# Performance work log

Hardware: AMD Instinct MI355X
Metric: run time of the kernel (lower is better)

## Reference

```python
import math
import jax, jax.numpy as jnp
import numpy as np

B, DIM, C, N = 1024, 512, 1000, 8
R = 0.05
WEIGHT_LAMBDA = 0.3
CN = C * N
TOPK = math.ceil(R * CN)  # 400


def setup_inputs() -> dict:
    key = jax.random.key(0)
    k1, k2, k3 = jax.random.split(key, 3)
    x = jax.random.normal(k1, (B, DIM), dtype=jnp.float32)
    # kaiming_uniform_(a=sqrt(5)) on a (DIM, CN) tensor: fan_in = CN (torch 2D fan_in = size(1)),
    # gain = sqrt(2/(1+a^2)) = sqrt(1/3), bound = gain * sqrt(3/fan_in)
    bound = math.sqrt(1.0 / 3.0) * math.sqrt(3.0 / CN)
    proxies = jax.random.uniform(k2, (DIM, CN), dtype=jnp.float32, minval=-bound, maxval=bound)
    target = jax.random.randint(k3, (B,), 0, C)
    return {"x": x, "proxies": proxies, "target": target}


def reference(x, proxies, target):
    instance_label = jnp.repeat(jnp.arange(C), N)  # (CN,)

    # F.normalize(Proxies, p=2, dim=0) with eps=1e-12 clamp
    norm = jnp.maximum(jnp.linalg.norm(proxies, axis=0, keepdims=True), 1e-12)
    centers = proxies / norm  # (DIM, CN)

    similarity = x @ centers  # (B, CN)

    positive_mask = (target[:, None] == instance_label[None, :]).astype(similarity.dtype)

    # topk over similarity boosted so all positives are included, then scatter 1s
    _, idx = jax.lax.top_k(similarity + 1000.0 * positive_mask, TOPK)  # (B, TOPK)
    mask = jnp.zeros_like(similarity).at[jnp.arange(B)[:, None], idx].set(1.0)
    mask = jax.lax.stop_gradient(mask)

    prob_a = mask * similarity  # (B, CN)
    # matmul with block one-hot y_instance_onehot == sum over the N proxies of each class
    logits = prob_a.reshape(B, C, N).sum(axis=-1)  # (B, C)

    logits_mask = jax.lax.stop_gradient((logits != 0.0).astype(logits.dtype))
    exp_l = jnp.exp(logits) * logits_mask
    predict = exp_l / (1e-8 + exp_l.sum(axis=1, keepdims=True))

    # sum(-y_onehot * log(predict+1e-20), 1) == -log(predict[b, target[b]] + 1e-20)
    loss_classify = jnp.mean(-jnp.log(predict[jnp.arange(B), target] + 1e-20))

    # regularizer: (centers.T @ centers) @ y_instance_onehot, fused as
    # centers.T @ (per-class sum of centers) -- identical math, avoids the CNxCN matrix
    centers_cls = centers.reshape(DIM, C, N).sum(axis=-1)  # (DIM, C)
    centers_logits = centers.T @ centers_cls  # (CN, C)
    logp = jax.nn.log_softmax(centers_logits, axis=1)
    reg = -jnp.mean(logp[jnp.arange(CN), instance_label])

    total = loss_classify + WEIGHT_LAMBDA * reg
    return (total, loss_classify)
```

## Files before the change

kernel.cpp:

```cpp
#include <hip/hip_runtime.h>
#include <hip/hip_bf16.h>
#include <math.h>

#define PB   1024
#define PDIM 512
#define PC   1000
#define PN   8
#define PCN  8000
#define PTOPK 400
#define NONPOS_K 392
#define NBIN 1024
#define CANDMAX 1024

typedef __bf16 bf16x8 __attribute__((ext_vector_type(8)));
typedef __bf16 bf16x4 __attribute__((ext_vector_type(4)));
typedef float  f32x4  __attribute__((ext_vector_type(4)));

__device__ static inline void async_load16(const __bf16* g, __bf16* l) {
    __builtin_amdgcn_global_load_lds(
        (const __attribute__((address_space(1))) void*)g,
        (__attribute__((address_space(3))) void*)l,
        16, 0, 0);
}

__global__ __launch_bounds__(256) void k_pre(const float* __restrict__ x,
                                             const float* __restrict__ P,
                                             __bf16* __restrict__ xb,
                                             float* __restrict__ ssqp,
                                             float* __restrict__ esd,
                                             float* __restrict__ padf,
                                             float* __restrict__ acc) {
    int b = blockIdx.x, tid = threadIdx.x;
    if (b == 0 && tid < 8) acc[tid] = 0.f;
    if (b < 512) {
        int i = b * 256 + tid;
        float4 v = ((const float4*)x)[i];
        bf16x4 o;
        o[0] = (__bf16)v.x; o[1] = (__bf16)v.y; o[2] = (__bf16)v.z; o[3] = (__bf16)v.w;
        ((bf16x4*)xb)[i] = o;
    } else if (b < 768) {
        int idx = b - 512;
        int slice = idx & 7, jb = idx >> 3;
        int j = jb * 256 + tid;
        if (j < PCN) {
            const float* p = P + (size_t)(slice * 64) * PCN + j;
            float ss = 0.f;
#pragma unroll 8
            for (int r = 0; r < 64; ++r) {
                float v = p[(size_t)r * PCN];
                ss = fmaf(v, v, ss);
            }
            ssqp[slice * PCN + j] = ss;
        }
    } else {
        int i = (b - 768) * 256 + tid;
        if (i < 16000) esd[i] = 0.f;
        else if (i < 16000 + 6144) padf[i - 16000] = 0.f;
    }
}

__global__ __launch_bounds__(256) void k_tpose(const float* __restrict__ P,
                                               const float* __restrict__ ssqp,
                                               __bf16* __restrict__ Pt,
                                               __bf16* __restrict__ ccls) {
    __shared__ float t[64][65];
    __shared__ float sinv[64];
    int tid = threadIdx.x;
    int tx = tid & 63, ty = tid >> 6;
    int j0 = blockIdx.x * 64, d0 = blockIdx.y * 64;
    if (tid < 64) {
        float sq = 0.f;
#pragma unroll
        for (int p2 = 0; p2 < 8; ++p2) sq += ssqp[p2 * PCN + j0 + tid];
        sinv[tid] = 1.0f / fmaxf(sqrtf(sq), 1e-12f);
    }
#pragma unroll
    for (int r = 0; r < 16; ++r) {
        int d = d0 + ty * 16 + r;
        t[ty * 16 + r][tx] = P[(size_t)d * PCN + j0 + tx];
    }
    __syncthreads();
    float cs0 = 0.f, cs1 = 0.f;
#pragma unroll
    for (int r = 0; r < 16; ++r) {
        int jl = ty * 16 + r;
        float val = t[tx][jl] * sinv[jl];
        Pt[(size_t)(j0 + jl) * PDIM + d0 + tx] = (__bf16)val;
        if (r < 8) cs0 += val; else cs1 += val;
    }
    int c0 = (j0 >> 3) + ty * 2;
    ccls[(size_t)c0 * PDIM + d0 + tx] = (__bf16)cs0;
    ccls[(size_t)(c0 + 1) * PDIM + d0 + tx] = (__bf16)cs1;
}

__global__ __launch_bounds__(512, 2) void k_gemms2(const __bf16* __restrict__ xb,
                                                   const __bf16* __restrict__ Pt,
                                                   const __bf16* __restrict__ ccls,
                                                   __bf16* __restrict__ simb,
                                                   float* __restrict__ esum,
                                                   float* __restrict__ diag) {
    __shared__ __align__(16) __bf16 As[2][256 * 64];
    __shared__ __align__(16) __bf16 Bs[2][256 * 64];

    int tid = threadIdx.x;
    int w = tid >> 6, lane = tid & 63;
    int wr = w >> 2, wc = w & 3;
    int quad = lane >> 4, l15 = lane & 15;

    int bid = blockIdx.x;
    bool is_sim = bid < 128;
    int M0, N0, Amax, Bmax;
    const __bf16 *Ab, *Bb;
    if (is_sim) {
        int mt = bid >> 5, nt = bid & 31;
        M0 = mt * 256; N0 = nt * 256;
        Ab = xb; Bb = Pt; Amax = PB - 1; Bmax = PCN - 1;
    } else {
        int b2 = bid - 128;
        int mt = b2 >> 2, nt = b2 & 3;
        M0 = mt * 256; N0 = nt * 256;
        Ab = Pt; Bb = ccls; Amax = PCN - 1; Bmax = 1023;
    }

    f32x4 acc[8][4] = {};

#define STAGE(kt_) {                                                         \
    int k0_ = (kt_) * 64, bb_ = (kt_) & 1;                                   \
    _Pragma("unroll")                                                        \
    for (int p_ = 0; p_ < 4; ++p_) {                                         \
        int idx_ = p_ * 512 + tid;                                           \
        int row_ = idx_ >> 3, sp_ = idx_ & 7;                                \
        int gk_ = ((sp_ ^ (row_ & 7)) << 3) + k0_;                           \
        int ga_ = M0 + row_; if (ga_ > Amax) ga_ = Amax;                     \
        async_load16(Ab + (size_t)ga_ * PDIM + gk_, &As[bb_][idx_ * 8]);     \
        int gb_ = N0 + row_; if (gb_ > Bmax) gb_ = Bmax;                     \
        async_load16(Bb + (size_t)gb_ * PDIM + gk_, &Bs[bb_][idx_ * 8]);     \
    } }

    STAGE(0)
    for (int kt = 0; kt < 8; ++kt) {
        int cur = kt & 1;
        asm volatile("s_waitcnt lgkmcnt(0)" ::: "memory");
        __builtin_amdgcn_s_barrier();
        if (kt < 7) {
            STAGE(kt + 1)
            asm volatile("s_waitcnt vmcnt(8)" ::: "memory");
        } else {
            asm volatile("s_waitcnt vmcnt(0)" ::: "memory");
        }
        __builtin_amdgcn_s_barrier();

#pragma unroll
        for (int ks = 0; ks < 2; ++ks) {
            bf16x8 af[8], bfr[4];
#pragma unroll
            for (int mi = 0; mi < 8; ++mi) {
                int row = wr * 128 + mi * 16 + l15;
                af[mi] = *(const bf16x8*)&As[cur][(row << 6) +
                         ((((ks << 2) + quad) ^ (row & 7)) << 3)];
            }
#pragma unroll
            for (int nj = 0; nj < 4; ++nj) {
                int row = wc * 64 + nj * 16 + l15;
                bfr[nj] = *(const bf16x8*)&Bs[cur][(row << 6) +
                          ((((ks << 2) + quad) ^ (row & 7)) << 3)];
            }
            __builtin_amdgcn_s_setprio(1);
#pragma unroll
            for (int mi = 0; mi < 8; ++mi)
#pragma unroll
                for (int nj = 0; nj < 4; ++nj)
                    acc[mi][nj] = __builtin_amdgcn_mfma_f32_16x16x32_bf16(
                        af[mi], bfr[nj], acc[mi][nj], 0, 0, 0);
            __builtin_amdgcn_s_setprio(0);
        }
    }
#undef STAGE

    if (is_sim) {
#pragma unroll
        for (int mi = 0; mi < 8; ++mi) {
            int r0 = M0 + wr * 128 + mi * 16 + quad * 4;
#pragma unroll
            for (int nj = 0; nj < 4; ++nj) {
                int cc = N0 + wc * 64 + nj * 16 + l15;
                if (cc < PCN) {
#pragma unroll
                    for (int r = 0; r < 4; ++r)
                        simb[(size_t)(r0 + r) * PCN + cc] = (__bf16)acc[mi][nj][r];
                }
            }
        }
    } else {
#pragma unroll
        for (int mi = 0; mi < 8; ++mi) {
            int r0 = M0 + wr * 128 + mi * 16 + quad * 4;
            float psum[4] = {0.f, 0.f, 0.f, 0.f};
#pragma unroll
            for (int nj = 0; nj < 4; ++nj) {
                int cc = N0 + wc * 64 + nj * 16 + l15;
                bool cvalid = (cc < PC);
#pragma unroll
                for (int r = 0; r < 4; ++r) {
                    float v = acc[mi][nj][r];
                    psum[r] += cvalid ? expf(v) : 0.f;
                    int rr = r0 + r;
                    if (cvalid && rr < PCN && cc == (rr >> 3)) diag[rr] = v;
                }
            }
#pragma unroll
            for (int off = 1; off < 16; off <<= 1)
#pragma unroll
                for (int r = 0; r < 4; ++r)
                    psum[r] += __shfl_xor(psum[r], off, 64);
            if (l15 == 0) {
#pragma unroll
                for (int r = 0; r < 4; ++r) {
                    int rr = r0 + r;
                    if (rr < PCN) atomicAdd(&esum[rr], psum[r]);
                }
            }
        }
    }
}

__global__ __launch_bounds__(256) void k_rowloss(const __bf16* __restrict__ sim,
                                                 const int* __restrict__ target,
                                                 float* __restrict__ acc) {
    __shared__ unsigned hist[NBIN];
    __shared__ float redf[8];
    __shared__ unsigned wtot[4];
    __shared__ float cand[CANDMAX];
    __shared__ unsigned candn;
    __shared__ int s_bin, s_A;
    __shared__ float s_tau;
    __shared__ int s_gt, s_eq;
    __shared__ float s_et;

    int b = blockIdx.x, tid = threadIdx.x;
    int lane = tid & 63, wv = tid >> 6;
    const bf16x8* row8 = (const bf16x8*)(sim + (size_t)b * PCN);
    int targ = target[b];

#pragma unroll
    for (int k = 0; k < 4; ++k) hist[tid + 256 * k] = 0u;
    if (tid == 0) candn = 0u;

    float pv[4][8];
    float lmn = INFINITY, lmx = -INFINITY;
#pragma unroll
    for (int k = 0; k < 4; ++k) {
        int c = tid + 256 * k;
        if (c < PC) {
            bf16x8 vv = row8[c];
#pragma unroll
            for (int n = 0; n < 8; ++n) pv[k][n] = (float)vv[n];
            if (c != targ) {
#pragma unroll
                for (int n = 0; n < 8; ++n) {
                    lmn = fminf(lmn, pv[k][n]);
                    lmx = fmaxf(lmx, pv[k][n]);
                }
            }
        } else {
#pragma unroll
            for (int n = 0; n < 8; ++n) pv[k][n] = 0.f;
        }
    }
    for (int off = 32; off; off >>= 1) {
        lmn = fminf(lmn, __shfl_down(lmn, off, 64));
        lmx = fmaxf(lmx, __shfl_down(lmx, off, 64));
    }
    if (lane == 0) { redf[wv] = lmn; redf[4 + wv] = lmx; }
    __syncthreads();
    float lo = fminf(fminf(redf[0], redf[1]), fminf(redf[2], redf[3]));
    float hi = fmaxf(fmaxf(redf[4], redf[5]), fmaxf(redf[6], redf[7]));
    float range = hi - lo;
    float scale = (range > 0.f) ? (float)NBIN / range : 0.f;

#pragma unroll
    for (int k = 0; k < 4; ++k) {
        int c = tid + 256 * k;
        if (c < PC && c != targ) {
#pragma unroll
            for (int n = 0; n < 8; ++n) {
                int bin = (int)((pv[k][n] - lo) * scale);
                bin = bin < 0 ? 0 : (bin > NBIN - 1 ? NBIN - 1 : bin);
                atomicAdd(&hist[bin], 1u);
            }
        }
    }
    __syncthreads();

    int b0 = tid * 4;
    unsigned h0 = hist[b0], h1 = hist[b0 + 1], h2 = hist[b0 + 2], h3 = hist[b0 + 3];
    unsigned l3 = h3, l2 = h2 + l3, l1 = h1 + l2, l0 = h0 + l1;
    unsigned T = l0;
#pragma unroll
    for (int step = 1; step < 64; step <<= 1) {
        unsigned u = __shfl_down(T, step, 64);
        if (lane + step < 64) T += u;
    }
    if (lane == 0) wtot[wv] = T;
    __syncthreads();
    unsigned tail = 0;
#pragma unroll
    for (int w2 = 0; w2 < 4; ++w2) if (w2 > wv) tail += wtot[w2];
    unsigned E = T - l0 + tail;
    {
        unsigned sfx[4] = {l0 + E, l1 + E, l2 + E, l3 + E};
        unsigned nxt[4] = {l1 + E, l2 + E, l3 + E, E};
#pragma unroll
        for (int i = 0; i < 4; ++i)
            if (sfx[i] >= NONPOS_K && nxt[i] < NONPOS_K) {
                s_bin = b0 + i;
                s_A = (int)nxt[i];
            }
    }
    __syncthreads();
    int tbin = s_bin, A = s_A;

#pragma unroll
    for (int k = 0; k < 4; ++k) {
        int c = tid + 256 * k;
        if (c < PC && c != targ) {
#pragma unroll
            for (int n = 0; n < 8; ++n) {
                int bin = (int)((pv[k][n] - lo) * scale);
                bin = bin < 0 ? 0 : (bin > NBIN - 1 ? NBIN - 1 : bin);
                if (bin == tbin) {
                    unsigned idx = atomicAdd(&candn, 1u);
                    if (idx < CANDMAX) cand[idx] = pv[k][n];
                }
            }
        }
    }
    __syncthreads();
    int m = (int)candn; if (m > CANDMAX) m = CANDMAX;
    int rank = NONPOS_K - A;
    for (int ci = tid; ci < m; ci += 256) {
        float val = cand[ci];
        int g = 0, e = 0;
        for (int i = 0; i < m; ++i) {
            g += cand[i] > val;
            e += cand[i] == val;
        }
        if (g < rank && rank <= g + e) { s_tau = val; s_gt = g; s_eq = e; }
    }
    __syncthreads();
    float tau = s_tau;
    int cgt = A + s_gt, ceq = s_eq;
    int rem = NONPOS_K - cgt;
    bool all_eq = (rem >= ceq);

    int offs[4] = {0, 0, 0, 0};
    if (!all_eq) {
        unsigned chunk_base = 0;
#pragma unroll
        for (int k = 0; k < 4; ++k) {
            int c = tid + 256 * k;
            unsigned tn = 0;
            if (c < PC && c != targ) {
#pragma unroll
                for (int n = 0; n < 8; ++n) tn += (pv[k][n] == tau) ? 1u : 0u;
            }
            unsigned inc = tn;
#pragma unroll
            for (int step = 1; step < 64; step <<= 1) {
                unsigned u = __shfl_up(inc, step, 64);
                if (lane >= step) inc += u;
            }
            __syncthreads();
            if (lane == 63) wtot[wv] = inc;
            __syncthreads();
            unsigned base = 0;
#pragma unroll
            for (int w2 = 0; w2 < 4; ++w2) if (w2 < wv) base += wtot[w2];
            offs[k] = (int)(chunk_base + base + inc - tn);
            chunk_base += wtot[0] + wtot[1] + wtot[2] + wtot[3];
        }
    }

    float psum = 0.f;
#pragma unroll
    for (int k = 0; k < 4; ++k) {
        int c = tid + 256 * k;
        if (c >= PC) continue;
        float lg = 0.f;
        if (c == targ) {
#pragma unroll
            for (int n = 0; n < 8; ++n) lg += pv[k][n];
        } else {
#pragma unroll
            for (int n = 0; n < 8; ++n) {
                float v = pv[k][n];
                bool sel = v > tau;
                if (!sel && v == tau) {
                    if (all_eq) sel = true;
                    else { sel = (offs[k] < rem); offs[k]++; }
                }
                if (sel) lg += v;
            }
        }
        float e = (lg != 0.0f) ? expf(lg) : 0.0f;
        psum += e;
        if (c == targ) s_et = e;
    }
    for (int off = 32; off; off >>= 1) psum += __shfl_down(psum, off, 64);
    if (lane == 0) redf[wv] = psum;
    __syncthreads();
    if (tid == 0) {
        float denom = 1e-8f + redf[0] + redf[1] + redf[2] + redf[3];
        atomicAdd(acc, -logf(s_et / denom + 1e-20f));
    }
}

__global__ __launch_bounds__(256) void k_final(const float* __restrict__ esum,
                                               const float* __restrict__ diag,
                                               const float* __restrict__ acc,
                                               float* __restrict__ out) {
    __shared__ float redf[4];
    int tid = threadIdx.x, lane = tid & 63, wv = tid >> 6;
    float s = 0.f;
    for (int j = tid; j < PCN; j += 256)
        s += logf(esum[j]) - diag[j];
    for (int off = 32; off; off >>= 1) s += __shfl_down(s, off, 64);
    if (lane == 0) redf[wv] = s;
    __syncthreads();
    if (tid == 0) {
        float rg = (redf[0] + redf[1] + redf[2] + redf[3]) * (1.0f / PCN);
        float lc = acc[0] * (1.0f / PB);
        out[0] = lc + 0.3f * rg;
        out[1] = lc;
    }
}

extern "C" void kernel_launch(void* const* d_in, const int* in_sizes, int n_in,
                              void* d_out, int out_size, void* d_ws, size_t ws_size,
                              hipStream_t stream) {
    const float* x       = (const float*)d_in[0];
    const float* proxies = (const float*)d_in[1];
    const int*   target  = (const int*)d_in[2];
    float* out = (float*)d_out;
    float* ws  = (float*)d_ws;

    float*  acc   = ws;
    float*  ssqp  = ws + 64;
    float*  esum  = ws + 64064;
    float*  diag  = ws + 72064;
    __bf16* xb    = (__bf16*)(ws + 80064);
    __bf16* cclsb = (__bf16*)(ws + 342208);
    __bf16* Pt    = (__bf16*)(ws + 604352);
    __bf16* simb  = (__bf16*)(ws + 2652352);

    float* padf = (float*)cclsb + 256000;

    k_pre<<<856, 256, 0, stream>>>(x, proxies, xb, ssqp, esum, padf, acc);
    k_tpose<<<dim3(125, 8), 256, 0, stream>>>(proxies, ssqp, Pt, cclsb);

    k_gemms2<<<256, 512, 0, stream>>>(xb, Pt, cclsb, simb, esum, diag);

    k_rowloss<<<PB, 256, 0, stream>>>(simb, target, acc);
    k_final<<<1, 256, 0, stream>>>(esum, diag, acc, out);
}
```

Baseline: 138.6 us.

## Fuse prep kernels, pack bf16 sim stores, fold final reduction into rowloss

Merges the norm, transpose and convert kernels into one prep kernel, where each of 125 blocks computes the column norms for 64 proxies and then transposes all 8 DIM chunks itself. The final loss reduction moves into the last k_rowloss block through a completion counter, which removes a launch. GEMM similarity stores now pair adjacent bf16 values with a lane shuffle so each write is 32 bits. The trade-off is that the prep stage runs on only 125 blocks doing serial transpose work, which could become a bottleneck.

Result: slower. 203.3 us (+46.6%).

```diff
diff --git a/kernel.cpp b/kernel.cpp
--- a/kernel.cpp
+++ b/kernel.cpp
@@ -23,74 +23,75 @@
         16, 0, 0);
 }
 
-__global__ __launch_bounds__(256) void k_pre(const float* __restrict__ x,
-                                             const float* __restrict__ P,
-                                             __bf16* __restrict__ xb,
-                                             float* __restrict__ ssqp,
-                                             float* __restrict__ esd,
-                                             float* __restrict__ padf,
-                                             float* __restrict__ acc) {
-    int b = blockIdx.x, tid = threadIdx.x;
-    if (b == 0 && tid < 8) acc[tid] = 0.f;
-    if (b < 512) {
-        int i = b * 256 + tid;
+__device__ static inline unsigned bf16bits(float v) {
+    __bf16 b = (__bf16)v;
+    unsigned short u;
+    __builtin_memcpy(&u, &b, 2);
+    return (unsigned)u;
+}
+
+__global__ __launch_bounds__(256) void k_prep(const float* __restrict__ x,
+                                              const float* __restrict__ P,
+                                              __bf16* __restrict__ xb,
+                                              __bf16* __restrict__ Pt,
+                                              __bf16* __restrict__ ccls,
+                                              float* __restrict__ esd,
+                                              float* __restrict__ padf,
+                                              float* __restrict__ acc) {
+    int bid = blockIdx.x, tid = threadIdx.x;
+    if (bid < 125) {
+        __shared__ float t[64][65];
+        __shared__ float red[4][64];
+        __shared__ float sinv[64];
+        int j0 = bid * 64;
+        int tx = tid & 63, ty = tid >> 6;
+        {
+            const float* pc = P + (size_t)(ty * 128) * PCN + j0 + tx;
+            float ss = 0.f;
+#pragma unroll 8
+            for (int k = 0; k < 128; ++k) {
+                float v = pc[(size_t)k * PCN];
+                ss = fmaf(v, v, ss);
+            }
+            red[ty][tx] = ss;
+        }
+        __syncthreads();
+        if (tid < 64) {
+            float sq = red[0][tid] + red[1][tid] + red[2][tid] + red[3][tid];
+            sinv[tid] = 1.0f / fmaxf(sqrtf(sq), 1e-12f);
+        }
+        for (int dc = 0; dc < 8; ++dc) {
+            __syncthreads();
+#pragma unroll
+            for (int rr = 0; rr < 16; ++rr) {
+                int d = dc * 64 + ty * 16 + rr;
+                t[ty * 16 + rr][tx] = P[(size_t)d * PCN + j0 + tx];
+            }
+            __syncthreads();
+            float cs0 = 0.f, cs1 = 0.f;
+#pragma unroll
+            for (int rr = 0; rr < 16; ++rr) {
+                int jj = ty * 16 + rr;
+                float val = t[tx][jj] * sinv[jj];
+                Pt[(size_t)(j0 + jj) * PDIM + dc * 64 + tx] = (__bf16)val;
+                if (rr < 8) cs0 += val; else cs1 += val;
+            }
+            int c0 = (j0 >> 3) + ty * 2;
+            ccls[(size_t)c0 * PDIM + dc * 64 + tx] = (__bf16)cs0;
+            ccls[(size_t)(c0 + 1) * PDIM + dc * 64 + tx] = (__bf16)cs1;
+        }
+    } else if (bid < 637) {
+        int i = (bid - 125) * 256 + tid;
         float4 v = ((const float4*)x)[i];
         bf16x4 o;
         o[0] = (__bf16)v.x; o[1] = (__bf16)v.y; o[2] = (__bf16)v.z; o[3] = (__bf16)v.w;
         ((bf16x4*)xb)[i] = o;
-    } else if (b < 768) {
-        int idx = b - 512;
-        int slice = idx & 7, jb = idx >> 3;
-        int j = jb * 256 + tid;
-        if (j < PCN) {
-            const float* p = P + (size_t)(slice * 64) * PCN + j;
-            float ss = 0.f;
-#pragma unroll 8
-            for (int r = 0; r < 64; ++r) {
-                float v = p[(size_t)r * PCN];
-                ss = fmaf(v, v, ss);
-            }
-            ssqp[slice * PCN + j] = ss;
-        }
     } else {
-        int i = (b - 768) * 256 + tid;
+        if (bid == 637 && tid < 16) acc[tid] = 0.f;
+        int i = (bid - 637) * 256 + tid;
         if (i < 16000) esd[i] = 0.f;
         else if (i < 16000 + 6144) padf[i - 16000] = 0.f;
     }
-}
-
-__global__ __launch_bounds__(256) void k_tpose(const float* __restrict__ P,
-                                               const float* __restrict__ ssqp,
-                                               __bf16* __restrict__ Pt,
-                                               __bf16* __restrict__ ccls) {
-    __shared__ float t[64][65];
-    __shared__ float sinv[64];
-    int tid = threadIdx.x;
-    int tx = tid & 63, ty = tid >> 6;
-    int j0 = blockIdx.x * 64, d0 = blockIdx.y * 64;
-    if (tid < 64) {
-        float sq = 0.f;
-#pragma unroll
-        for (int p2 = 0; p2 < 8; ++p2) sq += ssqp[p2 * PCN + j0 + tid];
-        sinv[tid] = 1.0f / fmaxf(sqrtf(sq), 1e-12f);
-    }
-#pragma unroll
-    for (int r = 0; r < 16; ++r) {
-        int d = d0 + ty * 16 + r;
-        t[ty * 16 + r][tx] = P[(size_t)d * PCN + j0 + tx];
-    }
-    __syncthreads();
-    float cs0 = 0.f, cs1 = 0.f;
-#pragma unroll
-    for (int r = 0; r < 16; ++r) {
-        int jl = ty * 16 + r;
-        float val = t[tx][jl] * sinv[jl];
-        Pt[(size_t)(j0 + jl) * PDIM + d0 + tx] = (__bf16)val;
-        if (r < 8) cs0 += val; else cs1 += val;
-    }
-    int c0 = (j0 >> 3) + ty * 2;
-    ccls[(size_t)c0 * PDIM + d0 + tx] = (__bf16)cs0;
-    ccls[(size_t)(c0 + 1) * PDIM + d0 + tx] = (__bf16)cs1;
 }
 
 __global__ __launch_bounds__(512, 2) void k_gemms2(const __bf16* __restrict__ xb,
@@ -184,10 +185,12 @@
 #pragma unroll
             for (int nj = 0; nj < 4; ++nj) {
                 int cc = N0 + wc * 64 + nj * 16 + l15;
-                if (cc < PCN) {
-#pragma unroll
-                    for (int r = 0; r < 4; ++r)
-                        simb[(size_t)(r0 + r) * PCN + cc] = (__bf16)acc[mi][nj][r];
+#pragma unroll
+                for (int r = 0; r < 4; ++r) {
+                    unsigned p = bf16bits(acc[mi][nj][r]);
+                    unsigned q = (unsigned)__shfl_xor((int)p, 1, 64);
+                    if (((l15 & 1) == 0) && cc < PCN)
+                        *(unsigned*)&simb[(size_t)(r0 + r) * PCN + cc] = p | (q << 16);
                 }
             }
         }
@@ -226,7 +229,10 @@
 
 __global__ __launch_bounds__(256) void k_rowloss(const __bf16* __restrict__ sim,
                                                  const int* __restrict__ target,
-                                                 float* __restrict__ acc) {
+                                                 float* __restrict__ acc,
+                                                 const float* __restrict__ esum,
+                                                 const float* __restrict__ diag,
+                                                 float* __restrict__ out) {
     __shared__ unsigned hist[NBIN];
     __shared__ float redf[8];
     __shared__ unsigned wtot[4];
@@ -236,6 +242,7 @@
     __shared__ float s_tau;
     __shared__ int s_gt, s_eq;
     __shared__ float s_et;
+    __shared__ unsigned s_rank2;
 
     int b = blockIdx.x, tid = threadIdx.x;
     int lane = tid & 63, wv = tid >> 6;
@@ -413,25 +420,24 @@
         float denom = 1e-8f + redf[0] + redf[1] + redf[2] + redf[3];
         atomicAdd(acc, -logf(s_et / denom + 1e-20f));
     }
-}
-
-__global__ __launch_bounds__(256) void k_final(const float* __restrict__ esum,
-                                               const float* __restrict__ diag,
-                                               const float* __restrict__ acc,
-                                               float* __restrict__ out) {
-    __shared__ float redf[4];
-    int tid = threadIdx.x, lane = tid & 63, wv = tid >> 6;
-    float s = 0.f;
-    for (int j = tid; j < PCN; j += 256)
-        s += logf(esum[j]) - diag[j];
-    for (int off = 32; off; off >>= 1) s += __shfl_down(s, off, 64);
-    if (lane == 0) redf[wv] = s;
-    __syncthreads();
-    if (tid == 0) {
-        float rg = (redf[0] + redf[1] + redf[2] + redf[3]) * (1.0f / PCN);
-        float lc = acc[0] * (1.0f / PB);
-        out[0] = lc + 0.3f * rg;
-        out[1] = lc;
+
+    __threadfence();
+    if (tid == 0) s_rank2 = atomicAdd((unsigned*)(acc + 8), 1u);
+    __syncthreads();
+    if (s_rank2 == PB - 1) {
+        float s = 0.f;
+        for (int j = tid; j < PCN; j += 256)
+            s += logf(esum[j]) - diag[j];
+        for (int off = 32; off; off >>= 1) s += __shfl_down(s, off, 64);
+        __syncthreads();
+        if (lane == 0) redf[wv] = s;
+        __syncthreads();
+        if (tid == 0) {
+            float rg = (redf[0] + redf[1] + redf[2] + redf[3]) * (1.0f / PCN);
+            float lc = atomicAdd(acc, 0.0f) * (1.0f / PB);
+            out[0] = lc + 0.3f * rg;
+            out[1] = lc;
+        }
     }
 }
 
@@ -445,7 +451,6 @@
     float* ws  = (float*)d_ws;
 
     float*  acc   = ws;
-    float*  ssqp  = ws + 64;
     float*  esum  = ws + 64064;
     float*  diag  = ws + 72064;
     __bf16* xb    = (__bf16*)(ws + 80064);
@@ -455,11 +460,7 @@
 
     float* padf = (float*)cclsb + 256000;
 
-    k_pre<<<856, 256, 0, stream>>>(x, proxies, xb, ssqp, esum, padf, acc);
-    k_tpose<<<dim3(125, 8), 256, 0, stream>>>(proxies, ssqp, Pt, cclsb);
-
+    k_prep<<<725, 256, 0, stream>>>(x, proxies, xb, Pt, cclsb, esum, padf, acc);
     k_gemms2<<<256, 512, 0, stream>>>(xb, Pt, cclsb, simb, esum, diag);
-
-    k_rowloss<<<PB, 256, 0, stream>>>(simb, target, acc);
-    k_final<<<1, 256, 0, stream>>>(esum, diag, acc, out);
-}
+    k_rowloss<<<PB, 256, 0, stream>>>(simb, target, acc, esum, diag, out);
+}
```

## Use exact bf16 radix-key histogram for top-k threshold and pack sim stores

Applied to the files above, without the earlier changes.

Replaces the min/max-range float histogram with a two-level radix select over the 16-bit order-preserving key of bf16 values. This drops the min/max reduction and the O(m^2) candidate ranking loop. It also merges the four tie-offset prefix scans into one scan of packed 16-bit counts and switches expf to __expf. In the GEMM epilogue, adjacent bf16 similarity values are paired with a lane shuffle so each store writes 32 bits, halving the store count.

Result: no change. 140.5 us (+1.3%).

```diff
diff --git a/kernel.cpp b/kernel.cpp
--- a/kernel.cpp
+++ b/kernel.cpp
@@ -10,7 +10,6 @@
 #define PTOPK 400
 #define NONPOS_K 392
 #define NBIN 1024
-#define CANDMAX 1024
 
 typedef __bf16 bf16x8 __attribute__((ext_vector_type(8)));
 typedef __bf16 bf16x4 __attribute__((ext_vector_type(4)));
@@ -21,6 +20,26 @@
         (const __attribute__((address_space(1))) void*)g,
         (__attribute__((address_space(3))) void*)l,
         16, 0, 0);
+}
+
+__device__ static inline unsigned bf16bits(float v) {
+    __bf16 b = (__bf16)v;
+    unsigned short u;
+    __builtin_memcpy(&u, &b, 2);
+    return (unsigned)u;
+}
+
+__device__ static inline unsigned bkey(float v) {
+    unsigned u = bf16bits(v);
+    return (u & 0x8000u) ? ((~u) & 0xffffu) : (u | 0x8000u);
+}
+
+__device__ static inline float keyf(unsigned t) {
+    unsigned bits = (t & 0x8000u) ? ((t & 0x7fffu) << 16)
+                                  : ((~t & 0xffffu) << 16);
+    float f;
+    __builtin_memcpy(&f, &bits, 4);
+    return f;
 }
 
 __global__ __launch_bounds__(256) void k_pre(const float* __restrict__ x,
@@ -184,10 +203,12 @@
 #pragma unroll
             for (int nj = 0; nj < 4; ++nj) {
                 int cc = N0 + wc * 64 + nj * 16 + l15;
-                if (cc < PCN) {
-#pragma unroll
-                    for (int r = 0; r < 4; ++r)
-                        simb[(size_t)(r0 + r) * PCN + cc] = (__bf16)acc[mi][nj][r];
+#pragma unroll
+                for (int r = 0; r < 4; ++r) {
+                    unsigned p = bf16bits(acc[mi][nj][r]);
+                    unsigned q = (unsigned)__shfl_xor((int)p, 1, 64);
+                    if (((l15 & 1) == 0) && cc < PCN)
+                        *(unsigned*)&simb[(size_t)(r0 + r) * PCN + cc] = p | (q << 16);
                 }
             }
         }
@@ -228,13 +249,11 @@
                                                  const int* __restrict__ target,
                                                  float* __restrict__ acc) {
     __shared__ unsigned hist[NBIN];
-    __shared__ float redf[8];
+    __shared__ unsigned hist2[64];
+    __shared__ float redf[4];
     __shared__ unsigned wtot[4];
-    __shared__ float cand[CANDMAX];
-    __shared__ unsigned candn;
-    __shared__ int s_bin, s_A;
-    __shared__ float s_tau;
-    __shared__ int s_gt, s_eq;
+    __shared__ unsigned wtot2[4][2];
+    __shared__ unsigned s_cb, s_A, s_tauk, s_gt, s_eq;
     __shared__ float s_et;
 
     int b = blockIdx.x, tid = threadIdx.x;
@@ -244,52 +263,32 @@
 
 #pragma unroll
     for (int k = 0; k < 4; ++k) hist[tid + 256 * k] = 0u;
-    if (tid == 0) candn = 0u;
+    if (tid < 64) hist2[tid] = 0u;
 
     float pv[4][8];
-    float lmn = INFINITY, lmx = -INFINITY;
+    bool msk[4];
 #pragma unroll
     for (int k = 0; k < 4; ++k) {
         int c = tid + 256 * k;
+        msk[k] = (c < PC) && (c != targ);
         if (c < PC) {
             bf16x8 vv = row8[c];
 #pragma unroll
             for (int n = 0; n < 8; ++n) pv[k][n] = (float)vv[n];
-            if (c != targ) {
-#pragma unroll
-                for (int n = 0; n < 8; ++n) {
-                    lmn = fminf(lmn, pv[k][n]);
-                    lmx = fmaxf(lmx, pv[k][n]);
-                }
-            }
         } else {
 #pragma unroll
             for (int n = 0; n < 8; ++n) pv[k][n] = 0.f;
         }
     }
-    for (int off = 32; off; off >>= 1) {
-        lmn = fminf(lmn, __shfl_down(lmn, off, 64));
-        lmx = fmaxf(lmx, __shfl_down(lmx, off, 64));
-    }
-    if (lane == 0) { redf[wv] = lmn; redf[4 + wv] = lmx; }
-    __syncthreads();
-    float lo = fminf(fminf(redf[0], redf[1]), fminf(redf[2], redf[3]));
-    float hi = fmaxf(fmaxf(redf[4], redf[5]), fmaxf(redf[6], redf[7]));
-    float range = hi - lo;
-    float scale = (range > 0.f) ? (float)NBIN / range : 0.f;
-
-#pragma unroll
-    for (int k = 0; k < 4; ++k) {
-        int c = tid + 256 * k;
-        if (c < PC && c != targ) {
-#pragma unroll
-            for (int n = 0; n < 8; ++n) {
-                int bin = (int)((pv[k][n] - lo) * scale);
-                bin = bin < 0 ? 0 : (bin > NBIN - 1 ? NBIN - 1 : bin);
-                atomicAdd(&hist[bin], 1u);
-            }
-        }
-    }
+    __syncthreads();
+
+#pragma unroll
+    for (int k = 0; k < 4; ++k)
+        if (msk[k]) {
+#pragma unroll
+            for (int n = 0; n < 8; ++n)
+                atomicAdd(&hist[bkey(pv[k][n]) >> 6], 1u);
+        }
     __syncthreads();
 
     int b0 = tid * 4;
@@ -313,72 +312,78 @@
 #pragma unroll
         for (int i = 0; i < 4; ++i)
             if (sfx[i] >= NONPOS_K && nxt[i] < NONPOS_K) {
-                s_bin = b0 + i;
-                s_A = (int)nxt[i];
-            }
-    }
-    __syncthreads();
-    int tbin = s_bin, A = s_A;
-
-#pragma unroll
-    for (int k = 0; k < 4; ++k) {
-        int c = tid + 256 * k;
-        if (c < PC && c != targ) {
+                s_cb = (unsigned)(b0 + i);
+                s_A = nxt[i];
+            }
+    }
+    __syncthreads();
+    unsigned cb = s_cb, A = s_A;
+
+#pragma unroll
+    for (int k = 0; k < 4; ++k)
+        if (msk[k]) {
 #pragma unroll
             for (int n = 0; n < 8; ++n) {
-                int bin = (int)((pv[k][n] - lo) * scale);
-                bin = bin < 0 ? 0 : (bin > NBIN - 1 ? NBIN - 1 : bin);
-                if (bin == tbin) {
-                    unsigned idx = atomicAdd(&candn, 1u);
-                    if (idx < CANDMAX) cand[idx] = pv[k][n];
-                }
-            }
-        }
-    }
-    __syncthreads();
-    int m = (int)candn; if (m > CANDMAX) m = CANDMAX;
-    int rank = NONPOS_K - A;
-    for (int ci = tid; ci < m; ci += 256) {
-        float val = cand[ci];
-        int g = 0, e = 0;
-        for (int i = 0; i < m; ++i) {
-            g += cand[i] > val;
-            e += cand[i] == val;
-        }
-        if (g < rank && rank <= g + e) { s_tau = val; s_gt = g; s_eq = e; }
-    }
-    __syncthreads();
-    float tau = s_tau;
-    int cgt = A + s_gt, ceq = s_eq;
-    int rem = NONPOS_K - cgt;
-    bool all_eq = (rem >= ceq);
+                unsigned kk = bkey(pv[k][n]);
+                if ((kk >> 6) == cb) atomicAdd(&hist2[kk & 63u], 1u);
+            }
+        }
+    __syncthreads();
+
+    if (wv == 0) {
+        unsigned h = hist2[lane];
+        unsigned sfx = h;
+#pragma unroll
+        for (int step = 1; step < 64; step <<= 1) {
+            unsigned u = __shfl_down(sfx, step, 64);
+            if (lane + step < 64) sfx += u;
+        }
+        unsigned nxt = sfx - h;
+        if (A + sfx >= NONPOS_K && A + nxt < NONPOS_K) {
+            s_tauk = (cb << 6) | (unsigned)lane;
+            s_gt = A + nxt;
+            s_eq = h;
+        }
+    }
+    __syncthreads();
+    float tauf = keyf(s_tauk);
+    int rem = NONPOS_K - (int)s_gt;
+    bool all_eq = (rem >= (int)s_eq);
 
     int offs[4] = {0, 0, 0, 0};
     if (!all_eq) {
-        unsigned chunk_base = 0;
+        unsigned tn[4];
 #pragma unroll
         for (int k = 0; k < 4; ++k) {
-            int c = tid + 256 * k;
-            unsigned tn = 0;
-            if (c < PC && c != targ) {
-#pragma unroll
-                for (int n = 0; n < 8; ++n) tn += (pv[k][n] == tau) ? 1u : 0u;
-            }
-            unsigned inc = tn;
-#pragma unroll
-            for (int step = 1; step < 64; step <<= 1) {
-                unsigned u = __shfl_up(inc, step, 64);
-                if (lane >= step) inc += u;
-            }
-            __syncthreads();
-            if (lane == 63) wtot[wv] = inc;
-            __syncthreads();
-            unsigned base = 0;
-#pragma unroll
-            for (int w2 = 0; w2 < 4; ++w2) if (w2 < wv) base += wtot[w2];
-            offs[k] = (int)(chunk_base + base + inc - tn);
-            chunk_base += wtot[0] + wtot[1] + wtot[2] + wtot[3];
-        }
+            unsigned t = 0;
+            if (msk[k]) {
+#pragma unroll
+                for (int n = 0; n < 8; ++n) t += (pv[k][n] == tauf) ? 1u : 0u;
+            }
+            tn[k] = t;
+        }
+        unsigned p01 = tn[0] | (tn[1] << 16), p23 = tn[2] | (tn[3] << 16);
+        unsigned i01 = p01, i23 = p23;
+#pragma unroll
+        for (int step = 1; step < 64; step <<= 1) {
+            unsigned u0 = __shfl_up(i01, step, 64);
+            unsigned u1 = __shfl_up(i23, step, 64);
+            if (lane >= step) { i01 += u0; i23 += u1; }
+        }
+        if (lane == 63) { wtot2[wv][0] = i01; wtot2[wv][1] = i23; }
+        __syncthreads();
+        unsigned base01 = 0, base23 = 0, t01 = 0, t23 = 0;
+#pragma unroll
+        for (int w2 = 0; w2 < 4; ++w2) {
+            if (w2 < wv) { base01 += wtot2[w2][0]; base23 += wtot2[w2][1]; }
+            t01 += wtot2[w2][0]; t23 += wtot2[w2][1];
+        }
+        unsigned e01 = i01 - p01, e23 = i23 - p23;
+        unsigned tot0 = t01 & 0xffffu, tot1 = t01 >> 16, tot2 = t23 & 0xffffu;
+        offs[0] = (int)((base01 & 0xffffu) + (e01 & 0xffffu));
+        offs[1] = (int)(tot0 + (base01 >> 16) + (e01 >> 16));
+        offs[2] = (int)(tot0 + tot1 + (base23 & 0xffffu) + (e23 & 0xffffu));
+        offs[3] = (int)(tot0 + tot1 + tot2 + (base23 >> 16) + (e23 >> 16));
     }
 
     float psum = 0.f;
@@ -394,15 +399,15 @@
 #pragma unroll
             for (int n = 0; n < 8; ++n) {
                 float v = pv[k][n];
-                bool sel = v > tau;
-                if (!sel && v == tau) {
+                bool sel = v > tauf;
+                if (!sel && v == tauf) {
                     if (all_eq) sel = true;
                     else { sel = (offs[k] < rem); offs[k]++; }
                 }
                 if (sel) lg += v;
             }
         }
-        float e = (lg != 0.0f) ? expf(lg) : 0.0f;
+        float e = (lg != 0.0f) ? __expf(lg) : 0.0f;
         psum += e;
         if (c == targ) s_et = e;
     }
@@ -457,9 +462,7 @@
 
     k_pre<<<856, 256, 0, stream>>>(x, proxies, xb, ssqp, esum, padf, acc);
     k_tpose<<<dim3(125, 8), 256, 0, stream>>>(proxies, ssqp, Pt, cclsb);
-
     k_gemms2<<<256, 512, 0, stream>>>(xb, Pt, cclsb, simb, esum, diag);
-
     k_rowloss<<<PB, 256, 0, stream>>>(simb, target, acc);
     k_final<<<1, 256, 0, stream>>>(esum, diag, acc, out);
 }
```
